# Kernel tuning notes

Measured on AMD Instinct MI355X. Metric: run time of the kernel, lower is better.

Reference implementation:

```python
import jax, jax.numpy as jnp
import numpy as np
import math

WS = 12          # window side
N = WS * WS      # tokens per window = 144
C = 384          # channels
H = 12           # heads
NW = 4           # num windows per image (mask dim)
BW = 512         # total windows (num_windows * B)


def _rel_tables():
    # log-spaced continuous relative coords table, shape ((2*WS-1)^2, 2)
    r = np.arange(-(WS - 1), WS, dtype=np.float32)
    rc = np.stack(np.meshgrid(r, r, indexing='ij'), axis=-1)  # (2W-1, 2W-1, 2)
    rc = rc / (WS - 1) * WS
    table = np.sign(rc) * np.log2(np.abs(rc) + 1.0) / np.log2(8.0)
    # pairwise relative position index, shape (N, N)
    c = np.stack(np.meshgrid(np.arange(WS), np.arange(WS), indexing='ij')).reshape(2, -1)
    rel = (c[:, :, None] - c[:, None, :]).transpose(1, 2, 0)  # (N, N, 2)
    rel[..., 0] += WS - 1
    rel[..., 1] += WS - 1
    rel[..., 0] *= 2 * WS - 1
    idx = rel.sum(-1)
    return jnp.asarray(table.reshape(-1, 2)), jnp.asarray(idx)


def setup_inputs() -> dict:
    key = jax.random.key(0)
    ks = jax.random.split(key, 8)
    return {
        'x': jax.random.normal(ks[0], (BW, N, C), jnp.float32),
        'mask': jax.random.normal(ks[1], (NW, N, N), jnp.float32),
        'qkv_w': jax.random.normal(ks[2], (3 * C, C), jnp.float32) * 0.02,
        'qkv_b': jnp.zeros((3 * C,), jnp.float32),
        'logit_scale': jnp.log(10.0) * jnp.ones((H, 1, 1), jnp.float32),
        'cpb_w1': jax.random.normal(ks[3], (512, 2), jnp.float32) * 0.02,
        'cpb_b1': jnp.zeros((512,), jnp.float32),
        'cpb_w2': jax.random.normal(ks[4], (H, 512), jnp.float32) * 0.02,
        'proj_w': jax.random.normal(ks[5], (C, C), jnp.float32) * 0.02,
        'proj_b': jnp.zeros((C,), jnp.float32),
    }


def _l2norm(t):
    # F.normalize(dim=-1): divide by L2 norm clamped at 1e-12
    n = jnp.sqrt(jnp.sum(t * t, axis=-1, keepdims=True))
    return t / jnp.maximum(n, 1e-12)


def reference(x, mask, qkv_w, qkv_b, logit_scale, cpb_w1, cpb_b1, cpb_w2, proj_w, proj_b):
    table, idx = _rel_tables()
    B_, Nn, Cc = x.shape
    hd = Cc // H
    qkv = (x @ qkv_w.T + qkv_b).reshape(B_, Nn, 3, H, hd).transpose(2, 0, 3, 1, 4)
    q, k, v = qkv[0], qkv[1], qkv[2]  # each (B_, H, N, hd)

    # cosine attention with learned, clamped logit scale
    attn = jnp.einsum('bhnd,bhmd->bhnm', _l2norm(q), _l2norm(k))
    scale = jnp.exp(jnp.minimum(logit_scale, math.log(1.0 / 0.01)))  # (H,1,1)
    attn = attn * scale[None]

    # CPB-MLP relative position bias
    bias_tab = jax.nn.relu(table @ cpb_w1.T + cpb_b1) @ cpb_w2.T  # (529, H)
    bias = bias_tab[idx.reshape(-1)].reshape(Nn, Nn, H).transpose(2, 0, 1)
    attn = attn + 16.0 * jax.nn.sigmoid(bias)[None]

    # shifted-window mask add, then softmax
    num_win = mask.shape[0]
    attn = attn.reshape(B_ // num_win, num_win, H, Nn, Nn) + mask[None, :, None]
    attn = jax.nn.softmax(attn.reshape(B_, H, Nn, Nn), axis=-1)

    out = jnp.einsum('bhnm,bhmd->bnhd', attn, v).reshape(B_, Nn, Cc)
    return out @ proj_w.T + proj_b
```

## Files before the change

### kernel.cpp

```cpp
#include <hip/hip_runtime.h>
#include <hip/hip_fp16.h>


typedef _Float16 half8 __attribute__((ext_vector_type(8)));
typedef _Float16 half4v __attribute__((ext_vector_type(4)));
typedef float floatx4 __attribute__((ext_vector_type(4)));

#define BW 512
#define NTOK 144
#define CDIM 384
#define NH 12
#define HD 32
#define MROWS (BW * NTOK)
#define QKVN (3 * CDIM)

__device__ inline void llds16(const void* g, void* l) {
    __builtin_amdgcn_global_load_lds((const __attribute__((address_space(1))) void*)g,
                                     (__attribute__((address_space(3))) void*)l, 16, 0, 0);
}

__global__ __launch_bounds__(256) void cast_f2h(const float* __restrict__ s,
                                                _Float16* __restrict__ d, int n8) {
    int i = blockIdx.x * 256 + threadIdx.x;
    if (i >= n8) return;
    const float4* s4 = (const float4*)s;
    float4 a = s4[2 * i], b = s4[2 * i + 1];
    half8 h;
    h[0] = (_Float16)a.x; h[1] = (_Float16)a.y; h[2] = (_Float16)a.z; h[3] = (_Float16)a.w;
    h[4] = (_Float16)b.x; h[5] = (_Float16)b.y; h[6] = (_Float16)b.z; h[7] = (_Float16)b.w;
    ((half8*)d)[i] = h;
}

__global__ __launch_bounds__(256) void cast_weights(const float* __restrict__ w_qkv,
                                                    _Float16* __restrict__ qh,
                                                    const float* __restrict__ w_proj,
                                                    _Float16* __restrict__ ph) {
    const int nq = QKVN * CDIM / 8;
    const int np = CDIM * CDIM / 8;
    int i = blockIdx.x * 256 + threadIdx.x;
    const float4* s4; half8* d8; int j;
    if (i < nq) { s4 = (const float4*)w_qkv; d8 = (half8*)qh; j = i; }
    else if (i < nq + np) { s4 = (const float4*)w_proj; d8 = (half8*)ph; j = i - nq; }
    else return;
    float4 a = s4[2 * j], b = s4[2 * j + 1];
    half8 h;
    h[0] = (_Float16)a.x; h[1] = (_Float16)a.y; h[2] = (_Float16)a.z; h[3] = (_Float16)a.w;
    h[4] = (_Float16)b.x; h[5] = (_Float16)b.y; h[6] = (_Float16)b.z; h[7] = (_Float16)b.w;
    d8[j] = h;
}

__global__ void cpb_table(const float* __restrict__ w1, const float* __restrict__ b1,
                          const float* __restrict__ w2, float* __restrict__ tab) {
    int t = threadIdx.x;
    if (t >= 529) return;
    float u0 = (float)((t / 23) - 11) * (12.0f / 11.0f);
    float u1 = (float)((t % 23) - 11) * (12.0f / 11.0f);
    float x0 = copysignf(log2f(fabsf(u0) + 1.0f) * (1.0f / 3.0f), u0);
    float x1 = copysignf(log2f(fabsf(u1) + 1.0f) * (1.0f / 3.0f), u1);
    float acc[12] = {};
    for (int j = 0; j < 512; j++) {
        float hj = fmaf(x0, w1[2 * j], fmaf(x1, w1[2 * j + 1], b1[j]));
        hj = fmaxf(hj, 0.0f);
#pragma unroll
        for (int q = 0; q < 12; q++) acc[q] += hj * w2[q * 512 + j];
    }
    for (int q = 0; q < 12; q++) tab[t * 12 + q] = acc[q];
}

__global__ __launch_bounds__(256) void build_cm(const float* __restrict__ mask,
                                                const float* __restrict__ tab,
                                                float* __restrict__ CM) {
    int e = blockIdx.x * 256 + threadIdx.x;
    if (e >= 4 * NH * NTOK * NTOK) return;
    int j = e % NTOK; int r1 = e / NTOK;
    int i = r1 % NTOK; int r2 = r1 / NTOK;
    int h = r2 % NH;   int m = r2 / NH;
    int rt = ((i / 12) - (j / 12) + 11) * 23 + ((i % 12) - (j % 12) + 11);
    float bv = tab[rt * 12 + h];
    CM[e] = mask[m * (NTOK * NTOK) + i * NTOK + j] + 16.0f / (1.0f + __expf(-bv));
}

template <typename OutT>
__global__ __launch_bounds__(512) void gemm_bt(const _Float16* __restrict__ A,
                                               const _Float16* __restrict__ B,
                                               const float* __restrict__ bias,
                                               OutT* __restrict__ C, int M, int N, int K) {
    __shared__ __align__(16) _Float16 As[256 * 32];
    __shared__ __align__(16) _Float16 Bs[128 * 32];
    const int t = threadIdx.x;
    const int wv = t >> 6, l = t & 63;
    const int wm = wv >> 1, wn = wv & 1;
    const int lr = l & 15, lk = l >> 4;

    const int ntn = N >> 7;
    const int t8 = gridDim.x >> 3;
    const int tile = (blockIdx.x & 7) * t8 + (blockIdx.x >> 3);
    const long m0 = (long)(tile / ntn) * 256, n0 = (long)(tile % ntn) * 128;

    const int srow = t >> 2, scol = (t & 3) * 8;
    const _Float16* ag = A + (m0 + srow) * (long)K + scol;
    const _Float16* bg = B + (n0 + srow) * (long)K + scol;
    _Float16* asd = As + t * 8;
    _Float16* bsd = Bs + t * 8;

    floatx4 acc[4][4] = {};

    for (int k0 = 0; k0 < K; k0 += 32) {
        llds16(ag, asd);
        llds16(ag + 128 * (long)K, asd + 4096);
        llds16(bg, bsd);
        ag += 32; bg += 32;
        __syncthreads();
        half8 af[4], bf[4];
#pragma unroll
        for (int fi = 0; fi < 4; fi++)
            af[fi] = *(const half8*)&As[(wm * 64 + fi * 16 + lr) * 32 + lk * 8];
#pragma unroll
        for (int fj = 0; fj < 4; fj++)
            bf[fj] = *(const half8*)&Bs[(wn * 64 + fj * 16 + lr) * 32 + lk * 8];
#pragma unroll
        for (int fi = 0; fi < 4; fi++)
#pragma unroll
            for (int fj = 0; fj < 4; fj++)
                acc[fi][fj] = __builtin_amdgcn_mfma_f32_16x16x32_f16(af[fi], bf[fj], acc[fi][fj], 0, 0, 0);
        __syncthreads();
    }

#pragma unroll
    for (int fi = 0; fi < 4; fi++) {
        const long row = m0 + wm * 64 + fi * 16 + lk * 4;
#pragma unroll
        for (int fj = 0; fj < 4; fj++) {
            const long col = n0 + wn * 64 + fj * 16 + lr;
            const float bv = bias[col];
#pragma unroll
            for (int r = 0; r < 4; r++) {
                float v = acc[fi][fj][r] + bv;
                C[(row + r) * (long)N + col] = (OutT)v;
            }
        }
    }
}

__global__ __launch_bounds__(576) void attn_win(const _Float16* __restrict__ qkv,
                                                const float* __restrict__ CM,
                                                const float* __restrict__ lscale,
                                                _Float16* __restrict__ O) {
    __shared__ __align__(16) _Float16 Kn[NTOK * HD];
    __shared__ __align__(16) _Float16 Vt[HD * NTOK];
    __shared__ __align__(16) _Float16 P[9 * 16 * NTOK];

    const int bid = blockIdx.x;
    const int w = bid / NH, h = bid % NH;
    const int t = threadIdx.x;
    const int wv = t >> 6, l = t & 63;
    const int lr = l & 15, lk = l >> 4;

    const float sc = expf(fminf(lscale[h], 4.6051701859880914f));

    {
        const int row = t >> 2, part = t & 3;
        const size_t base = (size_t)(w * NTOK + row) * QKVN + h * HD + part * 8;
        half8 kv = *(const half8*)(qkv + base + CDIM);
        float ss = 0.f;
#pragma unroll
        for (int j = 0; j < 8; j++) { float f = (float)kv[j]; ss += f * f; }
        ss += __shfl_xor(ss, 1); ss += __shfl_xor(ss, 2);
        float inv = 1.0f / fmaxf(sqrtf(ss), 1e-12f);
        half8 kn;
#pragma unroll
        for (int j = 0; j < 8; j++) kn[j] = (_Float16)((float)kv[j] * inv);
        *(half8*)&Kn[row * HD + part * 8] = kn;

        half8 vv = *(const half8*)(qkv + base + 2 * CDIM);
#pragma unroll
        for (int j = 0; j < 8; j++) Vt[(part * 8 + j) * NTOK + row] = vv[j];
    }
    __syncthreads();

    half8 aq;
    {
        const size_t qb = (size_t)(w * NTOK + wv * 16 + lr) * QKVN + h * HD + lk * 8;
        half8 q = *(const half8*)(qkv + qb);
        float ss = 0.f;
#pragma unroll
        for (int j = 0; j < 8; j++) { float f = (float)q[j]; ss += f * f; }
        ss += __shfl_xor(ss, 16); ss += __shfl_xor(ss, 32);
        float inv = sc / fmaxf(sqrtf(ss), 1e-12f);
#pragma unroll
        for (int j = 0; j < 8; j++) aq[j] = (_Float16)((float)q[j] * inv);
    }

    floatx4 s[9];
#pragma unroll
    for (int cj = 0; cj < 9; cj++) {
        half8 bk = *(const half8*)&Kn[(cj * 16 + lr) * HD + lk * 8];
        floatx4 z = {};
        s[cj] = __builtin_amdgcn_mfma_f32_16x16x32_f16(aq, bk, z, 0, 0, 0);
    }
    const float* cmb = CM + (size_t)((w & 3) * NH + h) * (NTOK * NTOK)
                     + (wv * 16 + lk * 4) * NTOK + lr;
#pragma unroll
    for (int cj = 0; cj < 9; cj++)
#pragma unroll
        for (int r = 0; r < 4; r++) s[cj][r] += cmb[r * NTOK + cj * 16];

    float sm[4];
#pragma unroll
    for (int r = 0; r < 4; r++) {
        float m = s[0][r];
#pragma unroll
        for (int cj = 1; cj < 9; cj++) m = fmaxf(m, s[cj][r]);
        m = fmaxf(m, __shfl_xor(m, 1)); m = fmaxf(m, __shfl_xor(m, 2));
        m = fmaxf(m, __shfl_xor(m, 4)); m = fmaxf(m, __shfl_xor(m, 8));
        float sum = 0.f;
#pragma unroll
        for (int cj = 0; cj < 9; cj++) { s[cj][r] = __expf(s[cj][r] - m); sum += s[cj][r]; }
        sum += __shfl_xor(sum, 1); sum += __shfl_xor(sum, 2);
        sum += __shfl_xor(sum, 4); sum += __shfl_xor(sum, 8);
        sm[r] = sum;
    }

    _Float16* Pw = P + wv * 16 * NTOK;
#pragma unroll
    for (int cj = 0; cj < 9; cj++)
#pragma unroll
        for (int r = 0; r < 4; r++)
            Pw[(lk * 4 + r) * NTOK + cj * 16 + lr] = (_Float16)s[cj][r];

    floatx4 o0 = {}, o1 = {};
#pragma unroll
    for (int kb = 0; kb < 4; kb++) {
        half8 ap = *(const half8*)&Pw[lr * NTOK + kb * 32 + lk * 8];
        half8 b0 = *(const half8*)&Vt[lr * NTOK + kb * 32 + lk * 8];
        half8 b1 = *(const half8*)&Vt[(16 + lr) * NTOK + kb * 32 + lk * 8];
        o0 = __builtin_amdgcn_mfma_f32_16x16x32_f16(ap, b0, o0, 0, 0, 0);
        o1 = __builtin_amdgcn_mfma_f32_16x16x32_f16(ap, b1, o1, 0, 0, 0);
    }
    {
        half4v at  = *(const half4v*)&Pw[lr * NTOK + 128 + lk * 4];
        half4v bt0 = *(const half4v*)&Vt[lr * NTOK + 128 + lk * 4];
        half4v bt1 = *(const half4v*)&Vt[(16 + lr) * NTOK + 128 + lk * 4];
        o0 = __builtin_amdgcn_mfma_f32_16x16x16f16(at, bt0, o0, 0, 0, 0);
        o1 = __builtin_amdgcn_mfma_f32_16x16x16f16(at, bt1, o1, 0, 0, 0);
    }

    const size_t ob = (size_t)(w * NTOK + wv * 16 + lk * 4) * CDIM + h * HD;
#pragma unroll
    for (int r = 0; r < 4; r++) {
        float inv = 1.0f / sm[r];
        O[ob + r * CDIM + lr]      = (_Float16)(o0[r] * inv);
        O[ob + r * CDIM + 16 + lr] = (_Float16)(o1[r] * inv);
    }
}

extern "C" void kernel_launch(void* const* d_in, const int* in_sizes, int n_in,
                              void* d_out, int out_size, void* d_ws, size_t ws_size,
                              hipStream_t stream) {
    const float* x     = (const float*)d_in[0];
    const float* mask  = (const float*)d_in[1];
    const float* qkv_w = (const float*)d_in[2];
    const float* qkv_b = (const float*)d_in[3];
    const float* lsc   = (const float*)d_in[4];
    const float* cw1   = (const float*)d_in[5];
    const float* cb1   = (const float*)d_in[6];
    const float* cw2   = (const float*)d_in[7];
    const float* pw    = (const float*)d_in[8];
    const float* pb    = (const float*)d_in[9];
    (void)in_sizes; (void)n_in; (void)out_size; (void)ws_size;

    char* ws = (char*)d_ws;
    float*    tab  = (float*)(ws);
    float*    CM   = (float*)(ws + 25600);
    _Float16* qw_h = (_Float16*)(ws + 4006912);
    _Float16* pw_h = (_Float16*)(ws + 4891648);
    _Float16* x_h  = (_Float16*)(ws + 5186560);
    _Float16* qkvh = (_Float16*)(ws + 61809664);
    _Float16* o_h  = x_h;

    cast_f2h<<<(MROWS * CDIM / 8) / 256, 256, 0, stream>>>(x, x_h, MROWS * CDIM / 8);
    cast_weights<<<(QKVN * CDIM / 8 + CDIM * CDIM / 8 + 255) / 256, 256, 0, stream>>>(
        qkv_w, qw_h, pw, pw_h);
    cpb_table<<<1, 576, 0, stream>>>(cw1, cb1, cw2, tab);
    build_cm<<<(4 * NH * NTOK * NTOK + 255) / 256, 256, 0, stream>>>(mask, tab, CM);

    gemm_bt<_Float16><<<(QKVN / 128) * (MROWS / 256), 512, 0, stream>>>(
        x_h, qw_h, qkv_b, qkvh, MROWS, QKVN, CDIM);

    attn_win<<<BW * NH, 576, 0, stream>>>(qkvh, CM, lsc, o_h);

    gemm_bt<float><<<(CDIM / 128) * (MROWS / 256), 512, 0, stream>>>(
        o_h, pw_h, pb, (float*)d_out, MROWS, CDIM, CDIM);
}
```

Before: 539.1 us.

## Compute transposed scores so softmax stays in registers and skip LDS P round-trip

Swaps the MFMA operand order for QK^T so each lane holds one query row's scores. Row max and sum then need only two cross-lane shuffles, and the probabilities feed the PV MFMA directly from registers as the B operand. This removes the P shared-memory buffer and its store/load traffic. The combined mask/bias loads become float4 vector loads and the output is written as half4 vectors. The Q load/normalise is also moved before the barrier to overlap with K/V staging. PV now uses nine 16x16x16 MFMAs instead of four 16x16x32 plus one 16x16x16, which is more MFMA issues.

```diff
diff --git a/kernel.cpp b/kernel.cpp
--- a/kernel.cpp
+++ b/kernel.cpp
@@ -148,7 +148,6 @@
                                                 _Float16* __restrict__ O) {
     __shared__ __align__(16) _Float16 Kn[NTOK * HD];
     __shared__ __align__(16) _Float16 Vt[HD * NTOK];
-    __shared__ __align__(16) _Float16 P[9 * 16 * NTOK];
 
     const int bid = blockIdx.x;
     const int w = bid / NH, h = bid % NH;
@@ -176,7 +175,6 @@
 #pragma unroll
         for (int j = 0; j < 8; j++) Vt[(part * 8 + j) * NTOK + row] = vv[j];
     }
-    __syncthreads();
 
     half8 aq;
     {
@@ -190,68 +188,62 @@
 #pragma unroll
         for (int j = 0; j < 8; j++) aq[j] = (_Float16)((float)q[j] * inv);
     }
+    __syncthreads();
 
     floatx4 s[9];
 #pragma unroll
     for (int cj = 0; cj < 9; cj++) {
         half8 bk = *(const half8*)&Kn[(cj * 16 + lr) * HD + lk * 8];
         floatx4 z = {};
-        s[cj] = __builtin_amdgcn_mfma_f32_16x16x32_f16(aq, bk, z, 0, 0, 0);
+        s[cj] = __builtin_amdgcn_mfma_f32_16x16x32_f16(bk, aq, z, 0, 0, 0);
     }
     const float* cmb = CM + (size_t)((w & 3) * NH + h) * (NTOK * NTOK)
-                     + (wv * 16 + lk * 4) * NTOK + lr;
+                     + (size_t)(wv * 16 + lr) * NTOK + lk * 4;
+#pragma unroll
+    for (int cj = 0; cj < 9; cj++) {
+        float4 c4 = *(const float4*)(cmb + cj * 16);
+        s[cj][0] += c4.x; s[cj][1] += c4.y; s[cj][2] += c4.z; s[cj][3] += c4.w;
+    }
+
+    float m = s[0][0];
 #pragma unroll
     for (int cj = 0; cj < 9; cj++)
 #pragma unroll
-        for (int r = 0; r < 4; r++) s[cj][r] += cmb[r * NTOK + cj * 16];
-
-    float sm[4];
+        for (int r = 0; r < 4; r++) m = fmaxf(m, s[cj][r]);
+    m = fmaxf(m, __shfl_xor(m, 16)); m = fmaxf(m, __shfl_xor(m, 32));
+    float sum = 0.f;
+#pragma unroll
+    for (int cj = 0; cj < 9; cj++)
+#pragma unroll
+        for (int r = 0; r < 4; r++) { s[cj][r] = __expf(s[cj][r] - m); sum += s[cj][r]; }
+    sum += __shfl_xor(sum, 16); sum += __shfl_xor(sum, 32);
+    const float inv = 1.0f / sum;
+
+    half4v pa[9];
+#pragma unroll
+    for (int cj = 0; cj < 9; cj++) {
+        pa[cj][0] = (_Float16)s[cj][0]; pa[cj][1] = (_Float16)s[cj][1];
+        pa[cj][2] = (_Float16)s[cj][2]; pa[cj][3] = (_Float16)s[cj][3];
+    }
+
+    floatx4 o0 = {}, o1 = {};
+#pragma unroll
+    for (int cj = 0; cj < 9; cj++) {
+        half4v v0 = *(const half4v*)&Vt[lr * NTOK + cj * 16 + lk * 4];
+        half4v v1 = *(const half4v*)&Vt[(16 + lr) * NTOK + cj * 16 + lk * 4];
+        o0 = __builtin_amdgcn_mfma_f32_16x16x16f16(v0, pa[cj], o0, 0, 0, 0);
+        o1 = __builtin_amdgcn_mfma_f32_16x16x16f16(v1, pa[cj], o1, 0, 0, 0);
+    }
+
+    const size_t ob = (size_t)(w * NTOK + wv * 16 + lr) * CDIM + h * HD + lk * 4;
+    half4v r0, r1;
 #pragma unroll
     for (int r = 0; r < 4; r++) {
-        float m = s[0][r];
-#pragma unroll
-        for (int cj = 1; cj < 9; cj++) m = fmaxf(m, s[cj][r]);
-        m = fmaxf(m, __shfl_xor(m, 1)); m = fmaxf(m, __shfl_xor(m, 2));
-        m = fmaxf(m, __shfl_xor(m, 4)); m = fmaxf(m, __shfl_xor(m, 8));
-        float sum = 0.f;
-#pragma unroll
-        for (int cj = 0; cj < 9; cj++) { s[cj][r] = __expf(s[cj][r] - m); sum += s[cj][r]; }
-        sum += __shfl_xor(sum, 1); sum += __shfl_xor(sum, 2);
-        sum += __shfl_xor(sum, 4); sum += __shfl_xor(sum, 8);
-        sm[r] = sum;
-    }
-
-    _Float16* Pw = P + wv * 16 * NTOK;
-#pragma unroll
-    for (int cj = 0; cj < 9; cj++)
-#pragma unroll
-        for (int r = 0; r < 4; r++)
-            Pw[(lk * 4 + r) * NTOK + cj * 16 + lr] = (_Float16)s[cj][r];
-
-    floatx4 o0 = {}, o1 = {};
-#pragma unroll
-    for (int kb = 0; kb < 4; kb++) {
-        half8 ap = *(const half8*)&Pw[lr * NTOK + kb * 32 + lk * 8];
-        half8 b0 = *(const half8*)&Vt[lr * NTOK + kb * 32 + lk * 8];
-        half8 b1 = *(const half8*)&Vt[(16 + lr) * NTOK + kb * 32 + lk * 8];
-        o0 = __builtin_amdgcn_mfma_f32_16x16x32_f16(ap, b0, o0, 0, 0, 0);
-        o1 = __builtin_amdgcn_mfma_f32_16x16x32_f16(ap, b1, o1, 0, 0, 0);
-    }
-    {
-        half4v at  = *(const half4v*)&Pw[lr * NTOK + 128 + lk * 4];
-        half4v bt0 = *(const half4v*)&Vt[lr * NTOK + 128 + lk * 4];
-        half4v bt1 = *(const half4v*)&Vt[(16 + lr) * NTOK + 128 + lk * 4];
-        o0 = __builtin_amdgcn_mfma_f32_16x16x16f16(at, bt0, o0, 0, 0, 0);
-        o1 = __builtin_amdgcn_mfma_f32_16x16x16f16(at, bt1, o1, 0, 0, 0);
-    }
-
-    const size_t ob = (size_t)(w * NTOK + wv * 16 + lk * 4) * CDIM + h * HD;
-#pragma unroll
-    for (int r = 0; r < 4; r++) {
-        float inv = 1.0f / sm[r];
-        O[ob + r * CDIM + lr]      = (_Float16)(o0[r] * inv);
-        O[ob + r * CDIM + 16 + lr] = (_Float16)(o1[r] * inv);
-    }
+        r0[r] = (_Float16)(o0[r] * inv);
+        r1[r] = (_Float16)(o1[r] * inv);
+    }
+    *(half4v*)&O[ob] = r0;
+    *(half4v*)&O[ob + 16] = r1;
 }
 
 extern "C" void kernel_launch(void* const* d_in, const int* in_sizes, int n_in,
```

New measurement: 518.6 us. 3.8% less time.
